# Optimization experiments

Measured on AMD Instinct MI355X. Metric: run time of the kernel, lower is better.

## Reference

```python
import jax, jax.numpy as jnp
import numpy as np

B, D_IN, UNITS = 2048, 4096, 4096

def setup_inputs() -> dict:
    key = jax.random.key(0)
    k_x, k_m, k_w, k_b = jax.random.split(key, 4)
    x = jax.random.normal(k_x, (B, D_IN), dtype=jnp.float32)
    mask = jax.random.randint(k_m, (D_IN, UNITS), 0, 2).astype(jnp.float32)
    # glorot_uniform kernel
    limit = np.sqrt(6.0 / (D_IN + UNITS)).astype(np.float32)
    W = jax.random.uniform(k_w, (D_IN, UNITS), dtype=jnp.float32, minval=-limit, maxval=limit)
    b = jnp.zeros((UNITS,), dtype=jnp.float32)
    return {"x": x, "mask": mask, "W": W, "b": b}

def reference(x, mask, W, b):
    # Original: build COO sparse tensor of kernel entries where mask != 0,
    # then (sparse_W^T @ x^T)^T == x @ (W masked by mask != 0). Bias added, no activation.
    W_masked = jnp.where(mask != 0.0, W, jnp.zeros((), dtype=W.dtype))
    return x @ W_masked + b
```

## Files before the change

### kernel.cpp

```cpp
#include <hip/hip_runtime.h>

#define M_DIM 2048
#define K_DIM 4096
#define N_DIM 4096
#define KTILES (K_DIM / 64)

typedef unsigned short u16;
typedef unsigned int u32;
typedef __bf16 bf16x8 __attribute__((ext_vector_type(8)));
typedef float f32x4 __attribute__((ext_vector_type(4)));
typedef float f4 __attribute__((ext_vector_type(4)));
typedef u16 u16x8 __attribute__((ext_vector_type(8)));
typedef u32 u32x4 __attribute__((ext_vector_type(4)));

__device__ __forceinline__ u16 f2bf(float f) {
    unsigned int u = __float_as_uint(f);
    u += 0x7fffu + ((u >> 16) & 1u);
    return (u16)(u >> 16);
}

__device__ __forceinline__ u32 pack2(float lo, float hi) {
    u32 a = __float_as_uint(lo); a += 0x7fffu + ((a >> 16) & 1u);
    u32 b = __float_as_uint(hi); b += 0x7fffu + ((b >> 16) & 1u);
    return (a >> 16) | (b & 0xffff0000u);
}

__device__ __forceinline__ void load16(const void* g, void* l) {
    __builtin_amdgcn_global_load_lds(
        (__attribute__((address_space(1))) const void*)g,
        (__attribute__((address_space(3))) void*)l,
        16, 0, 0);
}

__global__ __launch_bounds__(256) void prep_t(const float* __restrict__ W,
                                              const float* __restrict__ Msk,
                                              u16* __restrict__ Bt) {
    const int t = threadIdx.x;
    const int n0 = (blockIdx.x & 31) * 128;
    const int k0 = (blockIdx.x >> 5) * 64;
    const int ko = t & 7;
    const int ng = t >> 3;

    const float* Wp = W   + (size_t)(k0 + 8 * ko) * N_DIM + n0 + 4 * ng;
    const float* Mp = Msk + (size_t)(k0 + 8 * ko) * N_DIM + n0 + 4 * ng;

    f4 a[8];
#pragma unroll
    for (int j = 0; j < 8; ++j) {
        f4 wv = *(const f4*)(Wp + (size_t)j * N_DIM);
        f4 mv = *(const f4*)(Mp + (size_t)j * N_DIM);
        a[j][0] = mv[0] != 0.f ? wv[0] : 0.f;
        a[j][1] = mv[1] != 0.f ? wv[1] : 0.f;
        a[j][2] = mv[2] != 0.f ? wv[2] : 0.f;
        a[j][3] = mv[3] != 0.f ? wv[3] : 0.f;
    }

    u16* bp = Bt + (size_t)(n0 + 4 * ng) * K_DIM + k0 + 8 * ko;
#pragma unroll
    for (int i = 0; i < 4; ++i) {
        u32x4 o;
        o[0] = pack2(a[0][i], a[1][i]);
        o[1] = pack2(a[2][i], a[3][i]);
        o[2] = pack2(a[4][i], a[5][i]);
        o[3] = pack2(a[6][i], a[7][i]);
        *(u32x4*)(bp + (size_t)i * K_DIM) = o;
    }
}

__global__ __launch_bounds__(256) void prep_x(const float* __restrict__ x,
                                              u16* __restrict__ xb) {
    const int t = threadIdx.x;
    size_t i = ((size_t)blockIdx.x * 256 + t) * 16;
#pragma unroll
    for (int h = 0; h < 2; ++h) {
        f4 v0 = *(const f4*)(x + i + h * 8);
        f4 v1 = *(const f4*)(x + i + h * 8 + 4);
        u16x8 o;
        o[0] = f2bf(v0[0]); o[1] = f2bf(v0[1]); o[2] = f2bf(v0[2]); o[3] = f2bf(v0[3]);
        o[4] = f2bf(v1[0]); o[5] = f2bf(v1[1]); o[6] = f2bf(v1[2]); o[7] = f2bf(v1[3]);
        *(u16x8*)(xb + i + h * 8) = o;
    }
}

__global__ __launch_bounds__(512, 2) void gemm8(const u16* __restrict__ A,
                                                const u16* __restrict__ Bt,
                                                const float* __restrict__ bias,
                                                float* __restrict__ C) {
    __shared__ __align__(16) u16 As[3][128 * 64];
    __shared__ __align__(16) u16 Bs[3][256 * 64];

    const int t = threadIdx.x;
    const int wgid = blockIdx.x;
    const int xcd = wgid & 7, c = wgid >> 3;
    const int bm = (xcd & 1) * 8 + (c & 7);
    const int bn = (xcd >> 1) * 4 + (c >> 3);

    const int srow   = t >> 3;
    const int schunk = (t & 7) ^ (srow & 7);
    const u16* gA = A  + (size_t)(bm * 128 + srow) * K_DIM + schunk * 8;
    const u16* gB = Bt + (size_t)(bn * 256 + srow) * K_DIM + schunk * 8;

    const int lane = t & 63;
    const int wv   = t >> 6;
    const int kh = wv >> 2;
    const int wq = wv & 3;
    const int mo = (wq >> 1) * 64;
    const int no = (wq & 1) * 128;
    const int fr = lane & 15;
    const int q  = lane >> 4;
    const int sw = fr & 7;
    const int colK = (((kh << 2) + q) ^ sw) * 8;

#define SA(buf, kt, j) load16(gA + (size_t)(kt) * 64 + (size_t)(j) * 64 * K_DIM, \
                              (buf) + (j) * 4096 + t * 8)
#define SB(buf, kt, j) load16(gB + (size_t)(kt) * 64 + (size_t)(j) * 64 * K_DIM, \
                              (buf) + (j) * 4096 + t * 8)

    f32x4 acc[4][8] = {};

    u16 *aC = (u16*)As[0], *aN1 = (u16*)As[1], *aN2 = (u16*)As[2];
    u16 *bC = (u16*)Bs[0], *bN1 = (u16*)Bs[1], *bN2 = (u16*)Bs[2];

    SA(aC, 0, 0);  SA(aC, 0, 1);
    SB(bC, 0, 0);  SB(bC, 0, 1);  SB(bC, 0, 2);  SB(bC, 0, 3);
    SA(aN1, 1, 0); SA(aN1, 1, 1);
    SB(bN1, 1, 0); SB(bN1, 1, 1); SB(bN1, 1, 2); SB(bN1, 1, 3);
    asm volatile("s_waitcnt vmcnt(6)" ::: "memory");
    __builtin_amdgcn_sched_barrier(0);
    __builtin_amdgcn_s_barrier();

    for (int kt = 0; kt < KTILES; ++kt) {
        const int kn = (kt + 2) & (KTILES - 1);
        bf16x8 fA[4], fB0[4], fB1[4];

#pragma unroll
        for (int i = 0; i < 4; ++i)
            fA[i] = *(const bf16x8*)(aC + (mo + i * 16 + fr) * 64 + colK);
#pragma unroll
        for (int j = 0; j < 4; ++j)
            fB0[j] = *(const bf16x8*)(bC + (no + j * 16 + fr) * 64 + colK);
#pragma unroll
        for (int j = 0; j < 4; ++j)
            fB1[j] = *(const bf16x8*)(bC + (no + 64 + j * 16 + fr) * 64 + colK);

        asm volatile("s_waitcnt vmcnt(0)" ::: "memory");
        __builtin_amdgcn_sched_barrier(0);
        __builtin_amdgcn_s_barrier();

        SA(aN2, kn, 0); SA(aN2, kn, 1); SB(bN2, kn, 0);

        asm volatile("s_waitcnt lgkmcnt(4)" ::: "memory");
        __builtin_amdgcn_sched_barrier(0);
        __builtin_amdgcn_s_setprio(1);
#pragma unroll
        for (int i = 0; i < 4; ++i)
#pragma unroll
            for (int j = 0; j < 4; ++j)
                acc[i][j] = __builtin_amdgcn_mfma_f32_16x16x32_bf16(
                    fA[i], fB0[j], acc[i][j], 0, 0, 0);
        __builtin_amdgcn_s_setprio(0);
        asm volatile("s_waitcnt lgkmcnt(0)" ::: "memory");
        __builtin_amdgcn_sched_barrier(0);
        SB(bN2, kn, 1); SB(bN2, kn, 2); SB(bN2, kn, 3);
        __builtin_amdgcn_s_setprio(1);
#pragma unroll
        for (int i = 0; i < 4; ++i)
#pragma unroll
            for (int j = 0; j < 4; ++j)
                acc[i][j + 4] = __builtin_amdgcn_mfma_f32_16x16x32_bf16(
                    fA[i], fB1[j], acc[i][j + 4], 0, 0, 0);
        __builtin_amdgcn_s_setprio(0);

        u16* tmp;
        tmp = aC; aC = aN1; aN1 = aN2; aN2 = tmp;
        tmp = bC; bC = bN1; bN1 = bN2; bN2 = tmp;
    }

    asm volatile("s_waitcnt vmcnt(0)" ::: "memory");
    __builtin_amdgcn_s_barrier();

    float* red = (wq == 3) ? (float*)As : (float*)Bs[wq];

    if (kh == 1) {
#pragma unroll
        for (int i = 0; i < 4; ++i)
#pragma unroll
            for (int j = 0; j < 8; ++j)
                *(f32x4*)(red + (i * 8 + j) * 256 + lane * 4) = acc[i][j];
    }
    asm volatile("s_waitcnt lgkmcnt(0)" ::: "memory");
    __builtin_amdgcn_s_barrier();

    if (kh == 0) {
        const int rb = q * 4;
#pragma unroll
        for (int i = 0; i < 4; ++i) {
#pragma unroll
            for (int j = 0; j < 8; ++j) {
                f32x4 other = *(const f32x4*)(red + (i * 8 + j) * 256 + lane * 4);
                int n = bn * 256 + no + j * 16 + fr;
                float bv = bias[n];
#pragma unroll
                for (int r = 0; r < 4; ++r) {
                    int m = bm * 128 + mo + i * 16 + rb + r;
                    C[(size_t)m * N_DIM + n] = acc[i][j][r] + other[r] + bv;
                }
            }
        }
    }
#undef SA
#undef SB
}

extern "C" void kernel_launch(void* const* d_in, const int* in_sizes, int n_in,
                              void* d_out, int out_size, void* d_ws, size_t ws_size,
                              hipStream_t stream) {
    const float* x    = (const float*)d_in[0];
    const float* mask = (const float*)d_in[1];
    const float* W    = (const float*)d_in[2];
    const float* bias = (const float*)d_in[3];
    float* out = (float*)d_out;

    u16* Bt = (u16*)d_ws;
    u16* xb = (u16*)d_ws + (size_t)N_DIM * K_DIM;

    prep_t<<<2048, 256, 0, stream>>>(W, mask, Bt);
    prep_x<<<2048, 256, 0, stream>>>(x, xb);
    gemm8<<<256, 512, 0, stream>>>(xb, Bt, bias, out);
}
```

Before: 248.6 us.

## Load A fragments directly from global into registers, bypassing LDS

The A operand tiles are no longer staged through shared memory. Each wave loads its bf16 A fragments straight from global memory into registers one k-tile ahead, double-buffering them across a 2x unrolled loop. Only B is staged in LDS, with the shared buffer enlarged to four slots so the reduction scratch still fits. This removes LDS writes, reads and bandwidth pressure for A, but it duplicates A global loads across the waves that share rows and relies on global load latency being hidden by the one-tile register prefetch.

```diff
diff --git a/kernel.cpp b/kernel.cpp
--- a/kernel.cpp
+++ b/kernel.cpp
@@ -86,8 +86,7 @@
                                                 const u16* __restrict__ Bt,
                                                 const float* __restrict__ bias,
                                                 float* __restrict__ C) {
-    __shared__ __align__(16) u16 As[3][128 * 64];
-    __shared__ __align__(16) u16 Bs[3][256 * 64];
+    __shared__ __align__(16) u16 Bs[4][256 * 64];
 
     const int t = threadIdx.x;
     const int wgid = blockIdx.x;
@@ -97,7 +96,6 @@
 
     const int srow   = t >> 3;
     const int schunk = (t & 7) ^ (srow & 7);
-    const u16* gA = A  + (size_t)(bm * 128 + srow) * K_DIM + schunk * 8;
     const u16* gB = Bt + (size_t)(bn * 256 + srow) * K_DIM + schunk * 8;
 
     const int lane = t & 63;
@@ -111,75 +109,74 @@
     const int sw = fr & 7;
     const int colK = (((kh << 2) + q) ^ sw) * 8;
 
-#define SA(buf, kt, j) load16(gA + (size_t)(kt) * 64 + (size_t)(j) * 64 * K_DIM, \
-                              (buf) + (j) * 4096 + t * 8)
+    const u16* gAf = A + (size_t)(bm * 128 + mo + fr) * K_DIM + kh * 32 + q * 8;
+
 #define SB(buf, kt, j) load16(gB + (size_t)(kt) * 64 + (size_t)(j) * 64 * K_DIM, \
                               (buf) + (j) * 4096 + t * 8)
+#define LDA(dst, kt) do { \
+    _Pragma("unroll") \
+    for (int i_ = 0; i_ < 4; ++i_) \
+        dst[i_] = *(const bf16x8*)(gAf + (size_t)(i_ * 16) * K_DIM + (size_t)(kt) * 64); \
+    } while (0)
+
+#define BODY(kt, fAc, fAn) do { \
+    const int kn_ = ((kt) + 2) & (KTILES - 1); \
+    bf16x8 fB0[4], fB1[4]; \
+    _Pragma("unroll") \
+    for (int j_ = 0; j_ < 4; ++j_) \
+        fB0[j_] = *(const bf16x8*)(bC + (no + j_ * 16 + fr) * 64 + colK); \
+    _Pragma("unroll") \
+    for (int j_ = 0; j_ < 4; ++j_) \
+        fB1[j_] = *(const bf16x8*)(bC + (no + 64 + j_ * 16 + fr) * 64 + colK); \
+    LDA(fAn, ((kt) + 1) & (KTILES - 1)); \
+    asm volatile("s_waitcnt vmcnt(4)" ::: "memory"); \
+    __builtin_amdgcn_sched_barrier(0); \
+    __builtin_amdgcn_s_barrier(); \
+    SB(bN2, kn_, 0); SB(bN2, kn_, 1); SB(bN2, kn_, 2); SB(bN2, kn_, 3); \
+    asm volatile("s_waitcnt lgkmcnt(4)" ::: "memory"); \
+    __builtin_amdgcn_sched_barrier(0); \
+    __builtin_amdgcn_s_setprio(1); \
+    _Pragma("unroll") \
+    for (int i_ = 0; i_ < 4; ++i_) \
+        _Pragma("unroll") \
+        for (int j_ = 0; j_ < 4; ++j_) \
+            acc[i_][j_] = __builtin_amdgcn_mfma_f32_16x16x32_bf16( \
+                fAc[i_], fB0[j_], acc[i_][j_], 0, 0, 0); \
+    __builtin_amdgcn_s_setprio(0); \
+    asm volatile("s_waitcnt lgkmcnt(0)" ::: "memory"); \
+    __builtin_amdgcn_sched_barrier(0); \
+    __builtin_amdgcn_s_setprio(1); \
+    _Pragma("unroll") \
+    for (int i_ = 0; i_ < 4; ++i_) \
+        _Pragma("unroll") \
+        for (int j_ = 0; j_ < 4; ++j_) \
+            acc[i_][j_ + 4] = __builtin_amdgcn_mfma_f32_16x16x32_bf16( \
+                fAc[i_], fB1[j_], acc[i_][j_ + 4], 0, 0, 0); \
+    __builtin_amdgcn_s_setprio(0); \
+    u16* tmp_ = bC; bC = bN1; bN1 = bN2; bN2 = tmp_; \
+    } while (0)
 
     f32x4 acc[4][8] = {};
-
-    u16 *aC = (u16*)As[0], *aN1 = (u16*)As[1], *aN2 = (u16*)As[2];
+    bf16x8 fA_a[4], fA_b[4];
+
     u16 *bC = (u16*)Bs[0], *bN1 = (u16*)Bs[1], *bN2 = (u16*)Bs[2];
 
-    SA(aC, 0, 0);  SA(aC, 0, 1);
     SB(bC, 0, 0);  SB(bC, 0, 1);  SB(bC, 0, 2);  SB(bC, 0, 3);
-    SA(aN1, 1, 0); SA(aN1, 1, 1);
+    LDA(fA_a, 0);
     SB(bN1, 1, 0); SB(bN1, 1, 1); SB(bN1, 1, 2); SB(bN1, 1, 3);
-    asm volatile("s_waitcnt vmcnt(6)" ::: "memory");
+    asm volatile("s_waitcnt vmcnt(8)" ::: "memory");
     __builtin_amdgcn_sched_barrier(0);
     __builtin_amdgcn_s_barrier();
 
-    for (int kt = 0; kt < KTILES; ++kt) {
-        const int kn = (kt + 2) & (KTILES - 1);
-        bf16x8 fA[4], fB0[4], fB1[4];
-
-#pragma unroll
-        for (int i = 0; i < 4; ++i)
-            fA[i] = *(const bf16x8*)(aC + (mo + i * 16 + fr) * 64 + colK);
-#pragma unroll
-        for (int j = 0; j < 4; ++j)
-            fB0[j] = *(const bf16x8*)(bC + (no + j * 16 + fr) * 64 + colK);
-#pragma unroll
-        for (int j = 0; j < 4; ++j)
-            fB1[j] = *(const bf16x8*)(bC + (no + 64 + j * 16 + fr) * 64 + colK);
-
-        asm volatile("s_waitcnt vmcnt(0)" ::: "memory");
-        __builtin_amdgcn_sched_barrier(0);
-        __builtin_amdgcn_s_barrier();
-
-        SA(aN2, kn, 0); SA(aN2, kn, 1); SB(bN2, kn, 0);
-
-        asm volatile("s_waitcnt lgkmcnt(4)" ::: "memory");
-        __builtin_amdgcn_sched_barrier(0);
-        __builtin_amdgcn_s_setprio(1);
-#pragma unroll
-        for (int i = 0; i < 4; ++i)
-#pragma unroll
-            for (int j = 0; j < 4; ++j)
-                acc[i][j] = __builtin_amdgcn_mfma_f32_16x16x32_bf16(
-                    fA[i], fB0[j], acc[i][j], 0, 0, 0);
-        __builtin_amdgcn_s_setprio(0);
-        asm volatile("s_waitcnt lgkmcnt(0)" ::: "memory");
-        __builtin_amdgcn_sched_barrier(0);
-        SB(bN2, kn, 1); SB(bN2, kn, 2); SB(bN2, kn, 3);
-        __builtin_amdgcn_s_setprio(1);
-#pragma unroll
-        for (int i = 0; i < 4; ++i)
-#pragma unroll
-            for (int j = 0; j < 4; ++j)
-                acc[i][j + 4] = __builtin_amdgcn_mfma_f32_16x16x32_bf16(
-                    fA[i], fB1[j], acc[i][j + 4], 0, 0, 0);
-        __builtin_amdgcn_s_setprio(0);
-
-        u16* tmp;
-        tmp = aC; aC = aN1; aN1 = aN2; aN2 = tmp;
-        tmp = bC; bC = bN1; bN1 = bN2; bN2 = tmp;
+    for (int kt = 0; kt < KTILES; kt += 2) {
+        BODY(kt,     fA_a, fA_b);
+        BODY(kt + 1, fA_b, fA_a);
     }
 
     asm volatile("s_waitcnt vmcnt(0)" ::: "memory");
     __builtin_amdgcn_s_barrier();
 
-    float* red = (wq == 3) ? (float*)As : (float*)Bs[wq];
+    float* red = (float*)Bs[0] + (size_t)wq * (256 * 64 / 2);
 
     if (kh == 1) {
 #pragma unroll
@@ -208,8 +205,9 @@
             }
         }
     }
-#undef SA
 #undef SB
+#undef LDA
+#undef BODY
 }
 
 extern "C" void kernel_launch(void* const* d_in, const int* in_sizes, int n_in,
```

After: 280.2 us. 12.7% more time.
